# Performance work log

Measured on AMD Instinct MI355X. Metric: run time of the kernel, lower is better.

Reference implementation:

```python
import jax, jax.numpy as jnp
import numpy as np
from jax import lax

L = 41                                  # filter_length
H = 32                                  # hidden_size
XVALS = jnp.arange((-L) // 2, L // 2, dtype=jnp.float32)  # [-21, ..., 19], length 41 (matches torch.arange(-41//2, 41//2))


def _gauss_bank(mu, sig, C):
    # mu, sig, C: [H] -> filter bank [H, L]
    return C[:, None] * jnp.exp(-0.5 * ((XVALS[None, :] - mu[:, None]) / sig[:, None]) ** 2)


def _depthwise(z, filt):
    # z: [T, H], filt: [H, L] -> VALID cross-correlation per channel, [T-L+1, H]
    out = lax.conv_general_dilated(
        z.T[None],                      # [1, H, T] (NCH)
        filt[:, None, :],               # [H, 1, L] (OIH)
        window_strides=(1,), padding='VALID',
        feature_group_count=z.shape[1])
    return out[0].T


def setup_inputs() -> dict:
    key = jax.random.key(0)
    ks = jax.random.split(key, 8)
    T, D = 262144, 256
    x0 = jax.random.normal(ks[0], (T, 128), jnp.float32)
    x1 = jax.random.normal(ks[1], (T, 128), jnp.float32)
    W1 = jax.random.normal(ks[2], (H, D), jnp.float32) * 0.1   # fc1.weight [hidden, input]
    b1 = jax.random.normal(ks[3], (H,), jnp.float32) * 0.1     # fc1.bias
    V2 = jax.random.normal(ks[4], (D, H), jnp.float32)         # raw fc2 weight (Sphere-parametrized)
    b2 = jax.random.normal(ks[5], (D,), jnp.float32) * 0.1     # fc2.bias
    mus = jax.random.normal(ks[6], (2, H), jnp.float32) * 3.0
    sigmas = 1.0 + 2.0 * jax.random.uniform(ks[7], (2, H), jnp.float32)
    scaling = jnp.ones((2, H), jnp.float32)
    return {"x0": x0, "x1": x1, "W1": W1, "b1": b1, "V2": V2,
            "b2": b2, "mus": mus, "sigmas": sigmas, "scaling": scaling}


def reference(x0, x1, W1, b1, V2, b2, mus, sigmas, scaling):
    # Clamp (straight-through in bwd; forward value is clamp(min=1))
    std = jnp.clip(sigmas, 1.0, None)
    d = x0.shape[1]

    # ---- encode: per-region projection then per-channel Gaussian (flipped-mu) filters
    z0 = x0 @ W1[:, :d].T               # [T, H]
    z1 = x1 @ W1[:, d:].T               # [T, H]
    z = (_depthwise(z0, _gauss_bank(-mus[0], std[0], scaling[0]))
         + _depthwise(z1, _gauss_bank(-mus[1], std[1], scaling[1]))
         + b1)                          # [T-L+1, H]

    # ---- decode: Sphere-normalized readout (unit-norm columns of V2)
    W2 = V2 / jnp.linalg.norm(V2, axis=0, keepdims=True)  # [D, H]
    zd0 = _depthwise(z, _gauss_bank(mus[0], std[0], scaling[0]))  # [T-2L+2, H]
    zd1 = _depthwise(z, _gauss_bank(mus[1], std[1], scaling[1]))
    xh0 = zd0 @ W2[:d].T + b2[:d]       # [T-2L+2, d]
    xh1 = zd1 @ W2[d:].T + b2[d:]
    # model is untrained -> returns (zs dict, x_hats dict); flattened as tuple
    return (zd0, zd1, xh0, xh1)
```

## Files before the change

kernel.cpp:

```cpp
#include <hip/hip_runtime.h>
#include <math.h>

#define FL 41
#define NH 32
#define WS_E0  0
#define WS_E1  1312
#define WS_G0  2624
#define WS_G1  3936
#define WS_W2T 5248

__global__ __launch_bounds__(256) void setup_kernel(
    const float* __restrict__ V2, const float* __restrict__ mus,
    const float* __restrict__ sigmas, const float* __restrict__ scaling,
    float* __restrict__ ws)
{
    const int tid = threadIdx.x;
    __shared__ float nrm[NH];
    {
        const int h = tid >> 3;
        const int s = tid & 7;
        float p = 0.f;
        for (int jj = 0; jj < 32; ++jj) {
            const float v = V2[(s + jj*8)*NH + h];
            p += v*v;
        }
        p += __shfl_xor(p, 1, 8);
        p += __shfl_xor(p, 2, 8);
        p += __shfl_xor(p, 4, 8);
        if (s == 0) nrm[h] = sqrtf(p);
    }
    __syncthreads();
    for (int idx = tid; idx < NH*256; idx += 256) {
        int h = idx >> 8, j = idx & 255;
        ws[WS_W2T + idx] = V2[j*NH + h] / nrm[h];
    }
    for (int idx = tid; idx < 4*NH*FL; idx += 256) {
        int bank = idx / (NH*FL);
        int rem  = idx - bank*(NH*FL);
        int h = rem / FL, l = rem - h*FL;
        int r = bank & 1;
        float mu = mus[r*NH + h];
        float sg = fmaxf(sigmas[r*NH + h], 1.0f);
        float C  = scaling[r*NH + h];
        float m  = (bank < 2) ? -mu : mu;
        float x  = (float)(l - 21);
        float dd = (x - m) / sg;
        ws[idx] = C * expf(-0.5f * dd * dd);
    }
}

__global__ __launch_bounds__(256) void proj_kernel(
    const float* __restrict__ x0, const float* __restrict__ x1,
    const float* __restrict__ W1,
    float* __restrict__ z0, float* __restrict__ z1, int T)
{
    __shared__ float xT[2][32][132];
    __shared__ float wT[2][32][36];
    const int tid  = threadIdx.x;
    const int row0 = blockIdx.x * 128;

    const int reg = tid >> 7;
    const int h0  = ((tid >> 5) & 3) * 8;
    const int m   = tid & 31;

    float acc[4][8];
#pragma unroll
    for (int i = 0; i < 4; ++i)
#pragma unroll
        for (int j = 0; j < 8; ++j) acc[i][j] = 0.f;

    for (int kc = 0; kc < 4; ++kc) {
        const int c0 = kc * 32;
#pragma unroll
        for (int r = 0; r < 2; ++r) {
            const float* __restrict__ xp = r ? x1 : x0;
#pragma unroll
            for (int p = 0; p < 4; ++p) {
                const int row = p*32 + (tid >> 3);
                const int c   = (tid & 7) * 4;
                const float4 v = *reinterpret_cast<const float4*>(
                    &xp[(size_t)(row0 + row)*128 + c0 + c]);
                xT[r][c+0][row] = v.x; xT[r][c+1][row] = v.y;
                xT[r][c+2][row] = v.z; xT[r][c+3][row] = v.w;
            }
        }
        {
            const int h = tid >> 3;
            const int c = (tid & 7) * 4;
            const float4 a = *reinterpret_cast<const float4*>(&W1[h*256 + c0 + c]);
            wT[0][c+0][h] = a.x; wT[0][c+1][h] = a.y;
            wT[0][c+2][h] = a.z; wT[0][c+3][h] = a.w;
            const float4 b = *reinterpret_cast<const float4*>(&W1[h*256 + 128 + c0 + c]);
            wT[1][c+0][h] = b.x; wT[1][c+1][h] = b.y;
            wT[1][c+2][h] = b.z; wT[1][c+3][h] = b.w;
        }
        __syncthreads();
#pragma unroll
        for (int c = 0; c < 32; ++c) {
            const float4 xv = *reinterpret_cast<const float4*>(&xT[reg][c][m*4]);
            const float4 wa = *reinterpret_cast<const float4*>(&wT[reg][c][h0]);
            const float4 wb = *reinterpret_cast<const float4*>(&wT[reg][c][h0+4]);
            const float xs[4] = {xv.x, xv.y, xv.z, xv.w};
            const float wv[8] = {wa.x, wa.y, wa.z, wa.w, wb.x, wb.y, wb.z, wb.w};
#pragma unroll
            for (int i = 0; i < 4; ++i)
#pragma unroll
                for (int j = 0; j < 8; ++j) acc[i][j] += xs[i] * wv[j];
        }
        __syncthreads();
    }
    float* __restrict__ zp = reg ? z1 : z0;
#pragma unroll
    for (int i = 0; i < 4; ++i) {
        const size_t r = (size_t)(row0 + m*4 + i) * NH + h0;
        float4 o0 = make_float4(acc[i][0], acc[i][1], acc[i][2], acc[i][3]);
        float4 o1 = make_float4(acc[i][4], acc[i][5], acc[i][6], acc[i][7]);
        *reinterpret_cast<float4*>(&zp[r])   = o0;
        *reinterpret_cast<float4*>(&zp[r+4]) = o1;
    }
}

#define ED_BT 128
#define ED_RS 216
#define ED_ZR 176
__global__ __launch_bounds__(512) void encdec_kernel(
    const float* __restrict__ z0, const float* __restrict__ z1,
    const float* __restrict__ b1, const float* __restrict__ ws,
    float* __restrict__ zd0, float* __restrict__ zd1,
    int T, int T2)
{
    __shared__ float s0[ED_RS][NH];
    __shared__ float s1[ED_RS][NH];
    __shared__ float zt[ED_ZR][NH];
    const int tid = threadIdx.x;
    const int t0  = blockIdx.x * ED_BT;

    for (int idx = tid; idx < ED_RS*NH/4; idx += 512) {
        const int f = idx*4, row = f >> 5, col = f & 31;
        const int gr = t0 + row;
        float4 a = make_float4(0.f,0.f,0.f,0.f);
        float4 b = make_float4(0.f,0.f,0.f,0.f);
        if (gr < T) {
            a = *reinterpret_cast<const float4*>(&z0[(size_t)gr*NH + col]);
            b = *reinterpret_cast<const float4*>(&z1[(size_t)gr*NH + col]);
        }
        *reinterpret_cast<float4*>(&s0[row][col]) = a;
        *reinterpret_cast<float4*>(&s1[row][col]) = b;
    }
    __syncthreads();

    const int h = tid & 31;
    {
        const int g  = tid >> 5;
        const int tb = g * 11;
        float acc[11];
        const float bb = b1[h];
#pragma unroll
        for (int i = 0; i < 11; ++i) acc[i] = bb;
        float fr[FL];
#pragma unroll
        for (int l = 0; l < FL; ++l) fr[l] = ws[WS_E0 + h*FL + l];
#pragma unroll
        for (int s = 0; s < 51; ++s) {
            const float a0 = s0[tb + s][h];
#pragma unroll
            for (int i = 0; i < 11; ++i) {
                const int l = s - i;
                if (l >= 0 && l < FL) acc[i] += a0 * fr[l];
            }
        }
#pragma unroll
        for (int l = 0; l < FL; ++l) fr[l] = ws[WS_E1 + h*FL + l];
#pragma unroll
        for (int s = 0; s < 51; ++s) {
            const float a1 = s1[tb + s][h];
#pragma unroll
            for (int i = 0; i < 11; ++i) {
                const int l = s - i;
                if (l >= 0 && l < FL) acc[i] += a1 * fr[l];
            }
        }
#pragma unroll
        for (int i = 0; i < 11; ++i) zt[tb + i][h] = acc[i];
    }
    __syncthreads();

    {
        const int rr = (tid >> 5) & 1;
        const int g  = tid >> 6;
        const int tb = g * 16;
        float fr[FL];
        const float* __restrict__ fb = ws + (rr ? WS_G1 : WS_G0);
#pragma unroll
        for (int l = 0; l < FL; ++l) fr[l] = fb[h*FL + l];
        float acc[16];
#pragma unroll
        for (int i = 0; i < 16; ++i) acc[i] = 0.f;
#pragma unroll
        for (int s = 0; s < 56; ++s) {
            const float a = zt[tb + s][h];
#pragma unroll
            for (int i = 0; i < 16; ++i) {
                const int l = s - i;
                if (l >= 0 && l < FL) acc[i] += a * fr[l];
            }
        }
        float* __restrict__ zd = rr ? zd1 : zd0;
#pragma unroll
        for (int i = 0; i < 16; ++i) {
            const int t = t0 + tb + i;
            if (t < T2) zd[(size_t)t*NH + h] = acc[i];
        }
    }
}

#define RO_BT 128
__global__ __launch_bounds__(512) void readout_kernel(
    const float* __restrict__ zd0, const float* __restrict__ zd1,
    const float* __restrict__ W2T, const float* __restrict__ b2,
    float* __restrict__ xh0, float* __restrict__ xh1, int T2)
{
    __shared__ float w2[2][NH][132];
    __shared__ float sz[2][RO_BT][NH];
    const int tid = threadIdx.x;
    const int t0  = blockIdx.x * RO_BT;

    for (int idx = tid; idx < 2048; idx += 512) {
        const int h  = idx >> 6;
        const int jj = (idx & 63) * 4;
        const int r  = jj >> 7;
        const int j  = jj & 127;
        *reinterpret_cast<float4*>(&w2[r][h][j]) =
            *reinterpret_cast<const float4*>(&W2T[h*256 + jj]);
    }
    for (int idx = tid; idx < 2048; idx += 512) {
        const int f   = idx * 4;
        const int r   = f >> 12;
        const int rem = f & 4095;
        const int row = rem >> 5, col = rem & 31;
        const int t   = t0 + row;
        float4 v = make_float4(0.f, 0.f, 0.f, 0.f);
        if (t < T2) {
            const float* __restrict__ zp = r ? zd1 : zd0;
            v = *reinterpret_cast<const float4*>(&zp[(size_t)t*NH + col]);
        }
        *reinterpret_cast<float4*>(&sz[r][row][col]) = v;
    }
    __syncthreads();

    const int j  = (tid & 31) * 4;
    const int r  = (tid >> 5) & 1;
    const int rw = tid >> 6;

    float acc[16][4];
    {
        const float4 bv = *reinterpret_cast<const float4*>(&b2[r*128 + j]);
#pragma unroll
        for (int i = 0; i < 16; ++i) {
            acc[i][0] = bv.x; acc[i][1] = bv.y;
            acc[i][2] = bv.z; acc[i][3] = bv.w;
        }
    }

#pragma unroll 4
    for (int h = 0; h < NH; ++h) {
        const float4 w = *reinterpret_cast<const float4*>(&w2[r][h][j]);
#pragma unroll
        for (int i = 0; i < 16; ++i) {
            const float zv = sz[r][rw*16 + i][h];
            acc[i][0] += zv * w.x;
            acc[i][1] += zv * w.y;
            acc[i][2] += zv * w.z;
            acc[i][3] += zv * w.w;
        }
    }

    float* __restrict__ xp = r ? xh1 : xh0;
#pragma unroll
    for (int i = 0; i < 16; ++i) {
        const int t = t0 + rw*16 + i;
        if (t < T2) {
            float4 o = make_float4(acc[i][0], acc[i][1], acc[i][2], acc[i][3]);
            *reinterpret_cast<float4*>(&xp[(size_t)t*128 + j]) = o;
        }
    }
}

extern "C" void kernel_launch(void* const* d_in, const int* in_sizes, int n_in,
                              void* d_out, int out_size, void* d_ws, size_t ws_size,
                              hipStream_t stream)
{
    const float* x0      = (const float*)d_in[0];
    const float* x1      = (const float*)d_in[1];
    const float* W1      = (const float*)d_in[2];
    const float* b1      = (const float*)d_in[3];
    const float* V2      = (const float*)d_in[4];
    const float* b2      = (const float*)d_in[5];
    const float* mus     = (const float*)d_in[6];
    const float* sigmas  = (const float*)d_in[7];
    const float* scaling = (const float*)d_in[8];
    float* out = (float*)d_out;
    float* ws  = (float*)d_ws;

    const int T  = in_sizes[0] / 128;
    const int T2 = T - 80;

    float* zd0 = out;
    float* zd1 = out + (size_t)T2 * NH;
    float* xh0 = out + (size_t)2 * T2 * NH;
    float* xh1 = xh0 + (size_t)T2 * 128;

    float* z0 = xh0;
    float* z1 = xh0 + (size_t)T * NH;

    setup_kernel<<<1, 256, 0, stream>>>(V2, mus, sigmas, scaling, ws);
    proj_kernel<<<T / 128, 256, 0, stream>>>(x0, x1, W1, z0, z1, T);
    encdec_kernel<<<(T2 + ED_BT - 1) / ED_BT, 512, 0, stream>>>(
        z0, z1, b1, ws, zd0, zd1, T, T2);
    readout_kernel<<<(T2 + RO_BT - 1) / RO_BT, 512, 0, stream>>>(
        zd0, zd1, ws + WS_W2T, b2, xh0, xh1, T2);
}
```

Measured before the change: 647.5 us.

## Fuse projection with encode conv and decode conv with readout

Restructures the pipeline from three main kernels into two. The first fuses the x@W1 projection with the encode Gaussian convolution and writes only the single combined z to workspace. The second fuses the decode convolutions with the W2 readout, so zd is consumed from shared memory rather than re-read from global. This removes the z0/z1 intermediate round-trip and the zd reload, in exchange for recomputing halo rows (88 output rows per 128 projected) and for smaller per-block tiles.

Result: slower. 751.1 us (+16.0%).

```diff
diff --git a/kernel.cpp b/kernel.cpp
--- a/kernel.cpp
+++ b/kernel.cpp
@@ -8,6 +8,7 @@
 #define WS_G0  2624
 #define WS_G1  3936
 #define WS_W2T 5248
+#define WS_Z   16384
 
 __global__ __launch_bounds__(256) void setup_kernel(
     const float* __restrict__ V2, const float* __restrict__ mus,
@@ -49,23 +50,28 @@
     }
 }
 
-__global__ __launch_bounds__(256) void proj_kernel(
+#define PE_XR 128
+#define PE_ZB 88
+__global__ __launch_bounds__(512) void projenc_kernel(
     const float* __restrict__ x0, const float* __restrict__ x1,
-    const float* __restrict__ W1,
-    float* __restrict__ z0, float* __restrict__ z1, int T)
+    const float* __restrict__ W1, const float* __restrict__ b1,
+    const float* __restrict__ ws, float* __restrict__ z,
+    int T, int T1)
 {
     __shared__ float xT[2][32][132];
     __shared__ float wT[2][32][36];
-    const int tid  = threadIdx.x;
-    const int row0 = blockIdx.x * 128;
-
-    const int reg = tid >> 7;
-    const int h0  = ((tid >> 5) & 3) * 8;
-    const int m   = tid & 31;
-
-    float acc[4][8];
-#pragma unroll
-    for (int i = 0; i < 4; ++i)
+    __shared__ float s[2][PE_XR][33];
+    const int tid = threadIdx.x;
+    const int t0  = blockIdx.x * PE_ZB;
+
+    const int m  = tid & 63;
+    const int hq = (tid >> 6) & 3;
+    const int h0 = hq * 8;
+    const int rr = tid >> 8;
+
+    float acc[2][8];
+#pragma unroll
+    for (int i = 0; i < 2; ++i)
 #pragma unroll
         for (int j = 0; j < 8; ++j) acc[i][j] = 0.f;
 
@@ -75,156 +81,112 @@
         for (int r = 0; r < 2; ++r) {
             const float* __restrict__ xp = r ? x1 : x0;
 #pragma unroll
-            for (int p = 0; p < 4; ++p) {
-                const int row = p*32 + (tid >> 3);
+            for (int p = 0; p < 2; ++p) {
+                const int row = p*64 + (tid >> 3);
                 const int c   = (tid & 7) * 4;
-                const float4 v = *reinterpret_cast<const float4*>(
-                    &xp[(size_t)(row0 + row)*128 + c0 + c]);
+                const int gr  = t0 + row;
+                float4 v = make_float4(0.f, 0.f, 0.f, 0.f);
+                if (gr < T)
+                    v = *reinterpret_cast<const float4*>(
+                        &xp[(size_t)gr*128 + c0 + c]);
                 xT[r][c+0][row] = v.x; xT[r][c+1][row] = v.y;
                 xT[r][c+2][row] = v.z; xT[r][c+3][row] = v.w;
             }
         }
         {
-            const int h = tid >> 3;
-            const int c = (tid & 7) * 4;
-            const float4 a = *reinterpret_cast<const float4*>(&W1[h*256 + c0 + c]);
-            wT[0][c+0][h] = a.x; wT[0][c+1][h] = a.y;
-            wT[0][c+2][h] = a.z; wT[0][c+3][h] = a.w;
-            const float4 b = *reinterpret_cast<const float4*>(&W1[h*256 + 128 + c0 + c]);
-            wT[1][c+0][h] = b.x; wT[1][c+1][h] = b.y;
-            wT[1][c+2][h] = b.z; wT[1][c+3][h] = b.w;
+            const int h  = (tid >> 3) & 31;
+            const int wr = tid >> 8;
+            const int c  = (tid & 7) * 4;
+            const float4 a = *reinterpret_cast<const float4*>(
+                &W1[h*256 + wr*128 + c0 + c]);
+            wT[wr][c+0][h] = a.x; wT[wr][c+1][h] = a.y;
+            wT[wr][c+2][h] = a.z; wT[wr][c+3][h] = a.w;
         }
         __syncthreads();
 #pragma unroll
         for (int c = 0; c < 32; ++c) {
-            const float4 xv = *reinterpret_cast<const float4*>(&xT[reg][c][m*4]);
-            const float4 wa = *reinterpret_cast<const float4*>(&wT[reg][c][h0]);
-            const float4 wb = *reinterpret_cast<const float4*>(&wT[reg][c][h0+4]);
-            const float xs[4] = {xv.x, xv.y, xv.z, xv.w};
+            const float2 xv = *reinterpret_cast<const float2*>(&xT[rr][c][2*m]);
+            const float4 wa = *reinterpret_cast<const float4*>(&wT[rr][c][h0]);
+            const float4 wb = *reinterpret_cast<const float4*>(&wT[rr][c][h0+4]);
             const float wv[8] = {wa.x, wa.y, wa.z, wa.w, wb.x, wb.y, wb.z, wb.w};
 #pragma unroll
-            for (int i = 0; i < 4; ++i)
-#pragma unroll
-                for (int j = 0; j < 8; ++j) acc[i][j] += xs[i] * wv[j];
+            for (int j = 0; j < 8; ++j) {
+                acc[0][j] += xv.x * wv[j];
+                acc[1][j] += xv.y * wv[j];
+            }
         }
         __syncthreads();
     }
-    float* __restrict__ zp = reg ? z1 : z0;
-#pragma unroll
-    for (int i = 0; i < 4; ++i) {
-        const size_t r = (size_t)(row0 + m*4 + i) * NH + h0;
-        float4 o0 = make_float4(acc[i][0], acc[i][1], acc[i][2], acc[i][3]);
-        float4 o1 = make_float4(acc[i][4], acc[i][5], acc[i][6], acc[i][7]);
-        *reinterpret_cast<float4*>(&zp[r])   = o0;
-        *reinterpret_cast<float4*>(&zp[r+4]) = o1;
+#pragma unroll
+    for (int i = 0; i < 2; ++i)
+#pragma unroll
+        for (int j = 0; j < 8; ++j) s[rr][2*m + i][h0 + j] = acc[i][j];
+    __syncthreads();
+
+    {
+        const int h   = tid & 31;
+        const int grp = tid >> 5;
+        const int tb  = grp * 6;
+        float fa[6];
+        const float bb = b1[h];
+#pragma unroll
+        for (int i = 0; i < 6; ++i) fa[i] = bb;
+        float fr[FL];
+#pragma unroll
+        for (int l = 0; l < FL; ++l) fr[l] = ws[WS_E0 + h*FL + l];
+#pragma unroll
+        for (int ss = 0; ss < 46; ++ss) {
+            const int srow = tb + ss;
+            const float a0 = (srow < PE_XR) ? s[0][srow][h] : 0.f;
+#pragma unroll
+            for (int i = 0; i < 6; ++i) {
+                const int l = ss - i;
+                if (l >= 0 && l < FL) fa[i] += a0 * fr[l];
+            }
+        }
+#pragma unroll
+        for (int l = 0; l < FL; ++l) fr[l] = ws[WS_E1 + h*FL + l];
+#pragma unroll
+        for (int ss = 0; ss < 46; ++ss) {
+            const int srow = tb + ss;
+            const float a1 = (srow < PE_XR) ? s[1][srow][h] : 0.f;
+#pragma unroll
+            for (int i = 0; i < 6; ++i) {
+                const int l = ss - i;
+                if (l >= 0 && l < FL) fa[i] += a1 * fr[l];
+            }
+        }
+#pragma unroll
+        for (int i = 0; i < 6; ++i) {
+            const int t = t0 + tb + i;
+            if ((tb + i) < PE_ZB && t < T1) z[(size_t)t*NH + h] = fa[i];
+        }
     }
 }
 
-#define ED_BT 128
-#define ED_RS 216
-#define ED_ZR 176
-__global__ __launch_bounds__(512) void encdec_kernel(
-    const float* __restrict__ z0, const float* __restrict__ z1,
-    const float* __restrict__ b1, const float* __restrict__ ws,
+#define DR_BT 64
+#define DR_RS 104
+__global__ __launch_bounds__(512) void decread_kernel(
+    const float* __restrict__ z, const float* __restrict__ ws,
+    const float* __restrict__ W2T, const float* __restrict__ b2,
     float* __restrict__ zd0, float* __restrict__ zd1,
-    int T, int T2)
+    float* __restrict__ xh0, float* __restrict__ xh1,
+    int T1, int T2)
 {
-    __shared__ float s0[ED_RS][NH];
-    __shared__ float s1[ED_RS][NH];
-    __shared__ float zt[ED_ZR][NH];
+    __shared__ float sz[DR_RS][NH];
+    __shared__ float w2[2][NH][132];
+    __shared__ float zdl[2][DR_BT][NH];
     const int tid = threadIdx.x;
-    const int t0  = blockIdx.x * ED_BT;
-
-    for (int idx = tid; idx < ED_RS*NH/4; idx += 512) {
-        const int f = idx*4, row = f >> 5, col = f & 31;
-        const int gr = t0 + row;
-        float4 a = make_float4(0.f,0.f,0.f,0.f);
-        float4 b = make_float4(0.f,0.f,0.f,0.f);
-        if (gr < T) {
-            a = *reinterpret_cast<const float4*>(&z0[(size_t)gr*NH + col]);
-            b = *reinterpret_cast<const float4*>(&z1[(size_t)gr*NH + col]);
-        }
-        *reinterpret_cast<float4*>(&s0[row][col]) = a;
-        *reinterpret_cast<float4*>(&s1[row][col]) = b;
-    }
-    __syncthreads();
-
-    const int h = tid & 31;
-    {
-        const int g  = tid >> 5;
-        const int tb = g * 11;
-        float acc[11];
-        const float bb = b1[h];
-#pragma unroll
-        for (int i = 0; i < 11; ++i) acc[i] = bb;
-        float fr[FL];
-#pragma unroll
-        for (int l = 0; l < FL; ++l) fr[l] = ws[WS_E0 + h*FL + l];
-#pragma unroll
-        for (int s = 0; s < 51; ++s) {
-            const float a0 = s0[tb + s][h];
-#pragma unroll
-            for (int i = 0; i < 11; ++i) {
-                const int l = s - i;
-                if (l >= 0 && l < FL) acc[i] += a0 * fr[l];
-            }
-        }
-#pragma unroll
-        for (int l = 0; l < FL; ++l) fr[l] = ws[WS_E1 + h*FL + l];
-#pragma unroll
-        for (int s = 0; s < 51; ++s) {
-            const float a1 = s1[tb + s][h];
-#pragma unroll
-            for (int i = 0; i < 11; ++i) {
-                const int l = s - i;
-                if (l >= 0 && l < FL) acc[i] += a1 * fr[l];
-            }
-        }
-#pragma unroll
-        for (int i = 0; i < 11; ++i) zt[tb + i][h] = acc[i];
-    }
-    __syncthreads();
-
-    {
-        const int rr = (tid >> 5) & 1;
-        const int g  = tid >> 6;
-        const int tb = g * 16;
-        float fr[FL];
-        const float* __restrict__ fb = ws + (rr ? WS_G1 : WS_G0);
-#pragma unroll
-        for (int l = 0; l < FL; ++l) fr[l] = fb[h*FL + l];
-        float acc[16];
-#pragma unroll
-        for (int i = 0; i < 16; ++i) acc[i] = 0.f;
-#pragma unroll
-        for (int s = 0; s < 56; ++s) {
-            const float a = zt[tb + s][h];
-#pragma unroll
-            for (int i = 0; i < 16; ++i) {
-                const int l = s - i;
-                if (l >= 0 && l < FL) acc[i] += a * fr[l];
-            }
-        }
-        float* __restrict__ zd = rr ? zd1 : zd0;
-#pragma unroll
-        for (int i = 0; i < 16; ++i) {
-            const int t = t0 + tb + i;
-            if (t < T2) zd[(size_t)t*NH + h] = acc[i];
-        }
-    }
-}
-
-#define RO_BT 128
-__global__ __launch_bounds__(512) void readout_kernel(
-    const float* __restrict__ zd0, const float* __restrict__ zd1,
-    const float* __restrict__ W2T, const float* __restrict__ b2,
-    float* __restrict__ xh0, float* __restrict__ xh1, int T2)
-{
-    __shared__ float w2[2][NH][132];
-    __shared__ float sz[2][RO_BT][NH];
-    const int tid = threadIdx.x;
-    const int t0  = blockIdx.x * RO_BT;
-
+    const int t0  = blockIdx.x * DR_BT;
+
+    for (int idx = tid; idx < DR_RS*NH/4; idx += 512) {
+        const int row = idx >> 3, col = (idx & 7) * 4;
+        const int t   = t0 + row;
+        float4 v = make_float4(0.f, 0.f, 0.f, 0.f);
+        if (t < T1)
+            v = *reinterpret_cast<const float4*>(&z[(size_t)t*NH + col]);
+        *reinterpret_cast<float4*>(&sz[row][col]) = v;
+    }
     for (int idx = tid; idx < 2048; idx += 512) {
         const int h  = idx >> 6;
         const int jj = (idx & 63) * 4;
@@ -233,55 +195,73 @@
         *reinterpret_cast<float4*>(&w2[r][h][j]) =
             *reinterpret_cast<const float4*>(&W2T[h*256 + jj]);
     }
-    for (int idx = tid; idx < 2048; idx += 512) {
-        const int f   = idx * 4;
-        const int r   = f >> 12;
-        const int rem = f & 4095;
-        const int row = rem >> 5, col = rem & 31;
-        const int t   = t0 + row;
-        float4 v = make_float4(0.f, 0.f, 0.f, 0.f);
-        if (t < T2) {
-            const float* __restrict__ zp = r ? zd1 : zd0;
-            v = *reinterpret_cast<const float4*>(&zp[(size_t)t*NH + col]);
-        }
-        *reinterpret_cast<float4*>(&sz[r][row][col]) = v;
-    }
     __syncthreads();
 
-    const int j  = (tid & 31) * 4;
-    const int r  = (tid >> 5) & 1;
-    const int rw = tid >> 6;
-
-    float acc[16][4];
     {
-        const float4 bv = *reinterpret_cast<const float4*>(&b2[r*128 + j]);
-#pragma unroll
-        for (int i = 0; i < 16; ++i) {
-            acc[i][0] = bv.x; acc[i][1] = bv.y;
-            acc[i][2] = bv.z; acc[i][3] = bv.w;
-        }
-    }
-
+        const int h   = tid & 31;
+        const int rr  = (tid >> 5) & 1;
+        const int grp = tid >> 6;
+        const int tb  = grp * 8;
+        float fr[FL];
+        const float* __restrict__ fb = ws + (rr ? WS_G1 : WS_G0);
+#pragma unroll
+        for (int l = 0; l < FL; ++l) fr[l] = fb[h*FL + l];
+        float acc[8];
+#pragma unroll
+        for (int i = 0; i < 8; ++i) acc[i] = 0.f;
+#pragma unroll
+        for (int ss = 0; ss < 48; ++ss) {
+            const float a = sz[tb + ss][h];
+#pragma unroll
+            for (int i = 0; i < 8; ++i) {
+                const int l = ss - i;
+                if (l >= 0 && l < FL) acc[i] += a * fr[l];
+            }
+        }
+        float* __restrict__ zd = rr ? zd1 : zd0;
+#pragma unroll
+        for (int i = 0; i < 8; ++i) {
+            zdl[rr][tb + i][h] = acc[i];
+            const int t = t0 + tb + i;
+            if (t < T2) zd[(size_t)t*NH + h] = acc[i];
+        }
+    }
+    __syncthreads();
+
+    {
+        const int jl  = (tid & 31) * 4;
+        const int r   = (tid >> 5) & 1;
+        const int rw  = tid >> 6;
+        const int tb  = rw * 8;
+        float acc[8][4];
+        {
+            const float4 bv = *reinterpret_cast<const float4*>(&b2[r*128 + jl]);
+#pragma unroll
+            for (int i = 0; i < 8; ++i) {
+                acc[i][0] = bv.x; acc[i][1] = bv.y;
+                acc[i][2] = bv.z; acc[i][3] = bv.w;
+            }
+        }
 #pragma unroll 4
-    for (int h = 0; h < NH; ++h) {
-        const float4 w = *reinterpret_cast<const float4*>(&w2[r][h][j]);
-#pragma unroll
-        for (int i = 0; i < 16; ++i) {
-            const float zv = sz[r][rw*16 + i][h];
-            acc[i][0] += zv * w.x;
-            acc[i][1] += zv * w.y;
-            acc[i][2] += zv * w.z;
-            acc[i][3] += zv * w.w;
-        }
-    }
-
-    float* __restrict__ xp = r ? xh1 : xh0;
-#pragma unroll
-    for (int i = 0; i < 16; ++i) {
-        const int t = t0 + rw*16 + i;
-        if (t < T2) {
-            float4 o = make_float4(acc[i][0], acc[i][1], acc[i][2], acc[i][3]);
-            *reinterpret_cast<float4*>(&xp[(size_t)t*128 + j]) = o;
+        for (int h = 0; h < NH; ++h) {
+            const float4 w = *reinterpret_cast<const float4*>(&w2[r][h][jl]);
+#pragma unroll
+            for (int i = 0; i < 8; ++i) {
+                const float zv = zdl[r][tb + i][h];
+                acc[i][0] += zv * w.x;
+                acc[i][1] += zv * w.y;
+                acc[i][2] += zv * w.z;
+                acc[i][3] += zv * w.w;
+            }
+        }
+        float* __restrict__ xp = r ? xh1 : xh0;
+#pragma unroll
+        for (int i = 0; i < 8; ++i) {
+            const int t = t0 + tb + i;
+            if (t < T2) {
+                float4 o = make_float4(acc[i][0], acc[i][1], acc[i][2], acc[i][3]);
+                *reinterpret_cast<float4*>(&xp[(size_t)t*128 + jl]) = o;
+            }
         }
     }
 }
@@ -303,20 +283,18 @@
     float* ws  = (float*)d_ws;
 
     const int T  = in_sizes[0] / 128;
+    const int T1 = T - 40;
     const int T2 = T - 80;
 
     float* zd0 = out;
     float* zd1 = out + (size_t)T2 * NH;
     float* xh0 = out + (size_t)2 * T2 * NH;
     float* xh1 = xh0 + (size_t)T2 * 128;
-
-    float* z0 = xh0;
-    float* z1 = xh0 + (size_t)T * NH;
+    float* z   = ws + WS_Z;
 
     setup_kernel<<<1, 256, 0, stream>>>(V2, mus, sigmas, scaling, ws);
-    proj_kernel<<<T / 128, 256, 0, stream>>>(x0, x1, W1, z0, z1, T);
-    encdec_kernel<<<(T2 + ED_BT - 1) / ED_BT, 512, 0, stream>>>(
-        z0, z1, b1, ws, zd0, zd1, T, T2);
-    readout_kernel<<<(T2 + RO_BT - 1) / RO_BT, 512, 0, stream>>>(
-        zd0, zd1, ws + WS_W2T, b2, xh0, xh1, T2);
+    projenc_kernel<<<(T1 + PE_ZB - 1) / PE_ZB, 512, 0, stream>>>(
+        x0, x1, W1, b1, ws, z, T, T1);
+    decread_kernel<<<(T2 + DR_BT - 1) / DR_BT, 512, 0, stream>>>(
+        z, ws, ws + WS_W2T, b2, zd0, zd1, xh0, xh1, T1, T2);
 }
```
